# Optimization experiments

Measured on AMD Instinct MI355X. Metric: run time of the kernel, lower is better.

Reference implementation:

```python
import jax, jax.numpy as jnp
import numpy as np

WS = 8       # window_size
SHIFT = 4    # shift_size
NH = 6       # num_heads
C = 192      # dim
EPS = 1e-5


def _rel_index(ws):
    # standard Swin relative position index, [ws*ws, ws*ws]
    coords = np.stack(np.meshgrid(np.arange(ws), np.arange(ws), indexing='ij')).reshape(2, -1)
    rel = coords[:, :, None] - coords[:, None, :]            # [2, N, N]
    rel = rel.transpose(1, 2, 0) + (ws - 1)                  # shift to >= 0
    return rel[..., 0] * (2 * ws - 1) + rel[..., 1]          # [N, N]


def _attn_mask(h, w, ws, shift):
    # shifted-window attention mask, [nW, N, N] with 0 / -100
    img = np.zeros((h, w), dtype=np.float32)
    cnt = 0
    for hs in (slice(0, -ws), slice(-ws, -shift), slice(-shift, None)):
        for wsl in (slice(0, -ws), slice(-ws, -shift), slice(-shift, None)):
            img[hs, wsl] = cnt
            cnt += 1
    mw = img.reshape(h // ws, ws, w // ws, ws).transpose(0, 2, 1, 3).reshape(-1, ws * ws)
    diff = mw[:, None, :] - mw[:, :, None]
    return np.where(diff != 0, -100.0, 0.0).astype(np.float32)


def _ln(x, g, b):
    m = x.mean(-1, keepdims=True)
    v = ((x - m) ** 2).mean(-1, keepdims=True)
    return (x - m) / jnp.sqrt(v + EPS) * g + b


def setup_inputs() -> dict:
    key = jax.random.key(0)
    ks = jax.random.split(key, 16)
    B, H, W = 32, 64, 64
    Ch = 4 * C
    s = 0.02
    return {
        'x': jax.random.normal(ks[0], (B, H * W, C), jnp.float32),
        'h': H,
        'w': W,
        'norm1_g': jnp.ones((C,), jnp.float32),
        'norm1_b': jnp.zeros((C,), jnp.float32),
        'qkv_w': jax.random.normal(ks[1], (3 * C, C), jnp.float32) * s,
        'qkv_b': jnp.zeros((3 * C,), jnp.float32),
        'rpb_table': jax.random.normal(ks[2], ((2 * WS - 1) ** 2, NH), jnp.float32) * s,
        'proj_w': jax.random.normal(ks[3], (C, C), jnp.float32) * s,
        'proj_b': jnp.zeros((C,), jnp.float32),
        'norm2_g': jnp.ones((C,), jnp.float32),
        'norm2_b': jnp.zeros((C,), jnp.float32),
        'fc1_w': jax.random.normal(ks[4], (Ch, C), jnp.float32) * s,
        'fc1_b': jnp.zeros((Ch,), jnp.float32),
        'fc2_w': jax.random.normal(ks[5], (C, Ch), jnp.float32) * s,
        'fc2_b': jnp.zeros((C,), jnp.float32),
    }


def reference(x, h, w, norm1_g, norm1_b, qkv_w, qkv_b, rpb_table, proj_w, proj_b,
              norm2_g, norm2_b, fc1_w, fc1_b, fc2_w, fc2_b):
    B, L, _ = x.shape
    N = WS * WS
    hd = C // NH
    scale = hd ** -0.5
    nW = (h // WS) * (w // WS)

    shortcut = x
    xn = _ln(x, norm1_g, norm1_b).reshape(B, h, w, C)
    xs = jnp.roll(xn, (-SHIFT, -SHIFT), (1, 2))
    # window partition -> [B*nW, N, C]
    xw = xs.reshape(B, h // WS, WS, w // WS, WS, C).transpose(0, 1, 3, 2, 4, 5).reshape(-1, N, C)

    qkv = (xw @ qkv_w.T + qkv_b).reshape(-1, N, 3, NH, hd).transpose(2, 0, 3, 1, 4)
    q, k, v = qkv[0], qkv[1], qkv[2]                          # [B*nW, NH, N, hd]
    attn = jnp.einsum('whnd,whmd->whnm', q * scale, k)        # [B*nW, NH, N, N]
    bias = rpb_table[jnp.asarray(_rel_index(WS))].transpose(2, 0, 1)  # [NH, N, N]
    attn = attn + bias[None]
    mask = jnp.asarray(_attn_mask(h, w, WS, SHIFT))           # [nW, N, N]
    attn = attn.reshape(B, nW, NH, N, N) + mask[None, :, None]
    attn = jax.nn.softmax(attn.reshape(-1, NH, N, N), axis=-1)
    out = jnp.einsum('whnm,whmd->whnd', attn, v).transpose(0, 2, 1, 3).reshape(-1, N, C)
    out = out @ proj_w.T + proj_b

    # window reverse + unroll
    out = out.reshape(B, h // WS, w // WS, WS, WS, C).transpose(0, 1, 3, 2, 4, 5).reshape(B, h, w, C)
    out = jnp.roll(out, (SHIFT, SHIFT), (1, 2)).reshape(B, h * w, C)

    x = shortcut + out
    xn = _ln(x, norm2_g, norm2_b)
    mlp = jax.nn.gelu(xn @ fc1_w.T + fc1_b, approximate=False) @ fc2_w.T + fc2_b
    return x + mlp
```

## Files before the change

kernel.cpp:

```cpp
#include <hip/hip_runtime.h>
#include <hip/hip_bf16.h>
#include <math.h>

typedef __bf16 bf16;
typedef __bf16 bf16x8 __attribute__((ext_vector_type(8)));
typedef float f32x4 __attribute__((ext_vector_type(4)));

typedef const __attribute__((address_space(1))) char gchar;
typedef __attribute__((address_space(3))) char lchar;

#define BATCH 32
#define HW 64
#define L 4096
#define CDIM 192
#define NHEADS 6
#define HD 32
#define NTOK 131072
#define QKVC 576
#define CH 768

template <bool PERM, typename TIN>
__global__ __launch_bounds__(256) void ln_kernel(const TIN* __restrict__ xin,
                                                 const float* __restrict__ g,
                                                 const float* __restrict__ bta,
                                                 bf16* __restrict__ yout) {
  int wave = threadIdx.x >> 6;
  int lane = threadIdx.x & 63;
  int tok = blockIdx.x * 4 + wave;
  int src;
  if (PERM) {
    int win = tok >> 6;
    int n = tok & 63;
    int bb = win >> 6;
    int wid = win & 63;
    int i = ((wid >> 3) << 3) + (n >> 3);
    int j = ((wid & 7) << 3) + (n & 7);
    int sh = (i + 4) & 63;
    int sw = (j + 4) & 63;
    src = bb * L + sh * HW + sw;
  } else {
    src = tok;
  }
  const TIN* sp = xin + (size_t)src * CDIM;
  float v0 = (float)sp[lane];
  float v1 = (float)sp[lane + 64];
  float v2 = (float)sp[lane + 128];
  float s = v0 + v1 + v2;
#pragma unroll
  for (int off = 32; off; off >>= 1) s += __shfl_xor(s, off, 64);
  float mean = s * (1.0f / 192.0f);
  float d0 = v0 - mean, d1 = v1 - mean, d2 = v2 - mean;
  float q = d0 * d0 + d1 * d1 + d2 * d2;
#pragma unroll
  for (int off = 32; off; off >>= 1) q += __shfl_xor(q, off, 64);
  float rstd = rsqrtf(q * (1.0f / 192.0f) + 1e-5f);
  bf16* dp = yout + (size_t)tok * CDIM;
  dp[lane]       = (bf16)(d0 * rstd * g[lane]       + bta[lane]);
  dp[lane + 64]  = (bf16)(d1 * rstd * g[lane + 64]  + bta[lane + 64]);
  dp[lane + 128] = (bf16)(d2 * rstd * g[lane + 128] + bta[lane + 128]);
}

template <int EPI, typename TR, typename TO>
__global__ __launch_bounds__(256) void gemm_bt(const bf16* __restrict__ A,
                                               const float* __restrict__ W,
                                               const float* __restrict__ bias,
                                               const TR* __restrict__ res,
                                               TO* __restrict__ Cout,
                                               int M, int N, int K, int ldw) {
  __shared__ alignas(16) bf16 As[128 * 32];
  __shared__ alignas(16) bf16 Bs[64 * 32];
  const int n0 = blockIdx.x * 64;
  const int m0 = blockIdx.y * 128;
  const int tid = threadIdx.x;
  const int lane = tid & 63;
  const int wave = tid >> 6;
  const int wm = (wave >> 1) * 64;
  const int wn = (wave & 1) * 32;
  const int lr = lane & 15;
  const int quad = lane >> 4;

  f32x4 acc[4][2];
#pragma unroll
  for (int i = 0; i < 4; i++)
#pragma unroll
    for (int j = 0; j < 2; j++) acc[i][j] = (f32x4){0.f, 0.f, 0.f, 0.f};

  const int arow = tid >> 2;
  const int akq = (tid & 3) * 8;

  for (int k0 = 0; k0 < K; k0 += 32) {
    const bf16* Ap = A + (size_t)(m0 + arow) * K + k0 + akq;
    *(uint4*)(&As[arow * 32 + akq]) = *(const uint4*)Ap;
    *(uint4*)(&As[(arow + 64) * 32 + akq]) = *(const uint4*)(Ap + (size_t)64 * K);
    const float* Wp = W + (size_t)(n0 + arow) * ldw + k0 + akq;
    float4 w0 = *(const float4*)Wp;
    float4 w1 = *(const float4*)(Wp + 4);
    bf16x8 bw;
    bw[0] = (bf16)w0.x; bw[1] = (bf16)w0.y; bw[2] = (bf16)w0.z; bw[3] = (bf16)w0.w;
    bw[4] = (bf16)w1.x; bw[5] = (bf16)w1.y; bw[6] = (bf16)w1.z; bw[7] = (bf16)w1.w;
    *(bf16x8*)(&Bs[arow * 32 + akq]) = bw;
    __syncthreads();

    bf16x8 af[4], bfr[2];
#pragma unroll
    for (int mi = 0; mi < 4; mi++)
      af[mi] = *(const bf16x8*)(&As[(wm + mi * 16 + lr) * 32 + quad * 8]);
#pragma unroll
    for (int nj = 0; nj < 2; nj++)
      bfr[nj] = *(const bf16x8*)(&Bs[(wn + nj * 16 + lr) * 32 + quad * 8]);
#pragma unroll
    for (int mi = 0; mi < 4; mi++)
#pragma unroll
      for (int nj = 0; nj < 2; nj++)
        acc[mi][nj] = __builtin_amdgcn_mfma_f32_16x16x32_bf16(af[mi], bfr[nj],
                                                              acc[mi][nj], 0, 0, 0);
    __syncthreads();
  }

#pragma unroll
  for (int mi = 0; mi < 4; mi++) {
#pragma unroll
    for (int nj = 0; nj < 2; nj++) {
      int col = n0 + wn + nj * 16 + lr;
      float bv = bias[col];
#pragma unroll
      for (int r = 0; r < 4; r++) {
        int row = m0 + wm + mi * 16 + quad * 4 + r;
        float v = acc[mi][nj][r] + bv;
        size_t didx;
        if (EPI == 3) {
          int win = row >> 6, n = row & 63;
          int bb = win >> 6, wid = win & 63;
          int i = ((wid >> 3) << 3) + (n >> 3);
          int j = ((wid & 7) << 3) + (n & 7);
          int fi = (i + 4) & 63;
          int fj = (j + 4) & 63;
          didx = ((size_t)(bb * L + fi * HW + fj)) * (size_t)N + col;
          v += (float)res[didx];
        } else {
          didx = (size_t)row * N + col;
        }
        Cout[didx] = (TO)v;
      }
    }
  }
}

__device__ __forceinline__ int region64(int h) {
  return (h < 56) ? 0 : ((h < 60) ? 1 : 2);
}

__global__ __launch_bounds__(64) void attn_kernel(const bf16* __restrict__ qkv,
                                                  const float* __restrict__ rpb,
                                                  bf16* __restrict__ out) {
  __shared__ alignas(16) bf16 Qs[64 * 32];
  __shared__ alignas(16) bf16 Ks[64 * 32];
  __shared__ alignas(16) bf16 Vt[32 * 64];
  __shared__ alignas(16) bf16 Ps[64 * 64];
  const int win = blockIdx.x;
  const int head = blockIdx.y;
  const int lane = threadIdx.x;
  const int lr = lane & 15;
  const int quad = lane >> 4;
  const int wid = win & 63;
  const int wi = wid >> 3, wj = wid & 7;

  const bf16* base = qkv + (size_t)win * 64 * QKVC + head * HD;
#pragma unroll
  for (int rep = 0; rep < 4; rep++) {
    int r = (lane >> 2) + rep * 16;
    int c = (lane & 3) * 8;
    *(uint4*)(&Qs[r * 32 + c]) = *(const uint4*)(base + (size_t)r * QKVC + c);
    *(uint4*)(&Ks[r * 32 + c]) = *(const uint4*)(base + CDIM + (size_t)r * QKVC + c);
    uint4 vv = *(const uint4*)(base + 2 * CDIM + (size_t)r * QKVC + c);
    bf16x8 v8 = __builtin_bit_cast(bf16x8, vv);
#pragma unroll
    for (int j = 0; j < 8; j++) Vt[(c + j) * 64 + r] = v8[j];
  }
  __syncthreads();

  f32x4 s[4][4];
  {
    bf16x8 qf[4], kf[4];
#pragma unroll
    for (int mi = 0; mi < 4; mi++)
      qf[mi] = *(const bf16x8*)(&Qs[(mi * 16 + lr) * 32 + quad * 8]);
#pragma unroll
    for (int nj = 0; nj < 4; nj++)
      kf[nj] = *(const bf16x8*)(&Ks[(nj * 16 + lr) * 32 + quad * 8]);
#pragma unroll
    for (int mi = 0; mi < 4; mi++)
#pragma unroll
      for (int nj = 0; nj < 4; nj++)
        s[mi][nj] = __builtin_amdgcn_mfma_f32_16x16x32_bf16(
            qf[mi], kf[nj], (f32x4){0.f, 0.f, 0.f, 0.f}, 0, 0, 0);
  }

  const float scale = 0.17677669529663687f;
#pragma unroll
  for (int mi = 0; mi < 4; mi++) {
#pragma unroll
    for (int nj = 0; nj < 4; nj++) {
#pragma unroll
      for (int r = 0; r < 4; r++) {
        int rr = mi * 16 + quad * 4 + r;
        int cc = nj * 16 + lr;
        int qi = rr >> 3, qj = rr & 7, ki = cc >> 3, kj = cc & 7;
        int idx = (qi - ki + 7) * 15 + (qj - kj + 7);
        float bv = rpb[idx * NHEADS + head];
        int regr = 3 * region64(wi * 8 + qi) + region64(wj * 8 + qj);
        int regc = 3 * region64(wi * 8 + ki) + region64(wj * 8 + kj);
        float mv = (regr != regc) ? -100.0f : 0.0f;
        s[mi][nj][r] = s[mi][nj][r] * scale + bv + mv;
      }
    }
  }

#pragma unroll
  for (int mi = 0; mi < 4; mi++) {
#pragma unroll
    for (int r = 0; r < 4; r++) {
      float mx = s[mi][0][r];
#pragma unroll
      for (int nj = 1; nj < 4; nj++) mx = fmaxf(mx, s[mi][nj][r]);
#pragma unroll
      for (int off = 1; off < 16; off <<= 1) mx = fmaxf(mx, __shfl_xor(mx, off, 64));
      float sum = 0.f;
#pragma unroll
      for (int nj = 0; nj < 4; nj++) {
        float p = __expf(s[mi][nj][r] - mx);
        s[mi][nj][r] = p;
        sum += p;
      }
#pragma unroll
      for (int off = 1; off < 16; off <<= 1) sum += __shfl_xor(sum, off, 64);
      float inv = 1.0f / sum;
#pragma unroll
      for (int nj = 0; nj < 4; nj++) s[mi][nj][r] *= inv;
    }
  }

#pragma unroll
  for (int mi = 0; mi < 4; mi++)
#pragma unroll
    for (int nj = 0; nj < 4; nj++)
#pragma unroll
      for (int r = 0; r < 4; r++)
        Ps[(mi * 16 + quad * 4 + r) * 64 + nj * 16 + lr] = (bf16)s[mi][nj][r];
  __syncthreads();

  f32x4 o[4][2];
#pragma unroll
  for (int mi = 0; mi < 4; mi++)
#pragma unroll
    for (int nj = 0; nj < 2; nj++) o[mi][nj] = (f32x4){0.f, 0.f, 0.f, 0.f};
#pragma unroll
  for (int ks = 0; ks < 2; ks++) {
    bf16x8 pf[4], vf[2];
#pragma unroll
    for (int mi = 0; mi < 4; mi++)
      pf[mi] = *(const bf16x8*)(&Ps[(mi * 16 + lr) * 64 + ks * 32 + quad * 8]);
#pragma unroll
    for (int nj = 0; nj < 2; nj++)
      vf[nj] = *(const bf16x8*)(&Vt[(nj * 16 + lr) * 64 + ks * 32 + quad * 8]);
#pragma unroll
    for (int mi = 0; mi < 4; mi++)
#pragma unroll
      for (int nj = 0; nj < 2; nj++)
        o[mi][nj] = __builtin_amdgcn_mfma_f32_16x16x32_bf16(pf[mi], vf[nj],
                                                            o[mi][nj], 0, 0, 0);
  }

#pragma unroll
  for (int mi = 0; mi < 4; mi++)
#pragma unroll
    for (int nj = 0; nj < 2; nj++)
#pragma unroll
      for (int r = 0; r < 4; r++) {
        size_t row = (size_t)win * 64 + mi * 16 + quad * 4 + r;
        int col = head * HD + nj * 16 + lr;
        out[row * CDIM + col] = (bf16)o[mi][nj][r];
      }
}

__global__ __launch_bounds__(256) void wconv_kernel(const float* __restrict__ fc1w,
                                                    const float* __restrict__ fc2w,
                                                    bf16* __restrict__ W1b,
                                                    bf16* __restrict__ W2b) {
  int i = blockIdx.x * 256 + threadIdx.x;
  {
    int h = i / 192;
    int cc = i - h * 192;
    int gs = cc >> 3, e = cc & 7;
    int g = (gs & ~7) | ((gs & 7) ^ (h & 7));
    W1b[i] = (bf16)fc1w[h * 192 + g * 8 + e];
  }
  {
    int c = i / 12288;
    int rem = i - c * 12288;
    int n = rem >> 6;
    int cc = rem & 63;
    int gs = cc >> 3, e = cc & 7;
    int g = gs ^ (n & 7);
    W2b[i] = (bf16)fc2w[n * 768 + c * 64 + g * 8 + e];
  }
}

__global__ __launch_bounds__(512, 4) void mlp_fused(
    const bf16* __restrict__ Xn,
    const bf16* __restrict__ W1b,
    const bf16* __restrict__ W2b,
    const float* __restrict__ b1,
    const float* __restrict__ b2,
    const bf16* __restrict__ X1,
    float* __restrict__ out) {
  __shared__ alignas(16) bf16 W1s[64 * 192];
  __shared__ alignas(16) bf16 W2s[192 * 64];
  __shared__ alignas(16) bf16 Hs[8][16 * 64];

  const int tid = threadIdx.x;
  const int lane = tid & 63;
  const int wave = tid >> 6;
  const int lr = lane & 15;
  const int quad = lane >> 4;
  const int m0 = blockIdx.x * 128;
  const int arow = m0 + wave * 16 + lr;

  bf16x8 aF[6];
  {
    const bf16* ap = Xn + (size_t)arow * CDIM + quad * 8;
#pragma unroll
    for (int ks = 0; ks < 6; ks++)
      aF[ks] = *(const bf16x8*)(ap + ks * 32);
  }

  f32x4 oacc[12];
#pragma unroll
  for (int nt = 0; nt < 12; nt++) oacc[nt] = (f32x4){0.f, 0.f, 0.f, 0.f};

  for (int c = 0; c < 12; c++) {
    const int h0 = c * 64;
    {
      const size_t cb = (size_t)c * 24576;
      const int off = wave * 1024 + lane * 16;
      const char* g1 = (const char*)W1b + cb + off;
      const char* g2 = (const char*)W2b + cb + off;
      char* l1 = (char*)W1s + wave * 1024;
      char* l2 = (char*)W2s + wave * 1024;
#pragma unroll
      for (int i = 0; i < 3; i++) {
        __builtin_amdgcn_global_load_lds((gchar*)(g1 + i * 8192),
                                         (lchar*)(l1 + i * 8192), 16, 0, 0);
        __builtin_amdgcn_global_load_lds((gchar*)(g2 + i * 8192),
                                         (lchar*)(l2 + i * 8192), 16, 0, 0);
      }
    }
    __syncthreads();

    f32x4 hacc[4];
#pragma unroll
    for (int nj = 0; nj < 4; nj++) hacc[nj] = (f32x4){0.f, 0.f, 0.f, 0.f};
#pragma unroll
    for (int ks = 0; ks < 6; ks++) {
      int c8 = ks * 4 + quad;
      int base = (c8 & ~7) | ((c8 & 7) ^ (lr & 7));
#pragma unroll
      for (int nj = 0; nj < 4; nj++) {
        bf16x8 bF = *(const bf16x8*)(&W1s[(nj * 16 + lr) * 192 + base * 8]);
        hacc[nj] = __builtin_amdgcn_mfma_f32_16x16x32_bf16(aF[ks], bF, hacc[nj], 0, 0, 0);
      }
    }

#pragma unroll
    for (int nj = 0; nj < 4; nj++) {
      float bh = b1[h0 + nj * 16 + lr];
#pragma unroll
      for (int r = 0; r < 4; r++) {
        float h = hacc[nj][r] + bh;
        float x = fabsf(h) * 0.70710678118654752f;
        float t = __fdividef(1.0f, fmaf(0.3275911f, x, 1.0f));
        float p = t * (0.254829592f +
                  t * (-0.284496736f +
                  t * (1.421413741f +
                  t * (-1.453152027f + t * 1.061405429f))));
        float er = fmaf(-p, __expf(-x * x), 1.0f);
        er = copysignf(er, h);
        float gl = 0.5f * h * (1.0f + er);
        int hr = quad * 4 + r;
        int col = nj * 16 + lr;
        int c8 = col >> 3;
        int c8s = c8 ^ (hr & 7);
        Hs[wave][hr * 64 + c8s * 8 + (col & 7)] = (bf16)gl;
      }
    }

#pragma unroll
    for (int ks = 0; ks < 2; ks++) {
      int c8 = ks * 4 + quad;
      int c8s = c8 ^ (lr & 7);
      bf16x8 hF = *(const bf16x8*)(&Hs[wave][lr * 64 + c8s * 8]);
#pragma unroll
      for (int nt = 0; nt < 12; nt++) {
        bf16x8 wF = *(const bf16x8*)(&W2s[(nt * 16 + lr) * 64 + c8s * 8]);
        oacc[nt] = __builtin_amdgcn_mfma_f32_16x16x32_bf16(hF, wF, oacc[nt], 0, 0, 0);
      }
    }
    __syncthreads();
  }

#pragma unroll
  for (int nt = 0; nt < 12; nt++) {
    float fb = b2[nt * 16 + lr];
#pragma unroll
    for (int r = 0; r < 4; r++) {
      size_t row = (size_t)(m0 + wave * 16 + quad * 4 + r);
      size_t idx = row * CDIM + nt * 16 + lr;
      out[idx] = oacc[nt][r] + fb + (float)X1[idx];
    }
  }
}

extern "C" void kernel_launch(void* const* d_in, const int* in_sizes, int n_in,
                              void* d_out, int out_size, void* d_ws, size_t ws_size,
                              hipStream_t stream) {
  const float* x      = (const float*)d_in[0];
  const float* n1g    = (const float*)d_in[3];
  const float* n1b    = (const float*)d_in[4];
  const float* qkv_w  = (const float*)d_in[5];
  const float* qkv_b  = (const float*)d_in[6];
  const float* rpb    = (const float*)d_in[7];
  const float* proj_w = (const float*)d_in[8];
  const float* proj_b = (const float*)d_in[9];
  const float* n2g    = (const float*)d_in[10];
  const float* n2b    = (const float*)d_in[11];
  const float* fc1_w  = (const float*)d_in[12];
  const float* fc1_b  = (const float*)d_in[13];
  const float* fc2_w  = (const float*)d_in[14];
  const float* fc2_b  = (const float*)d_in[15];
  float* out = (float*)d_out;

  char* wsb = (char*)d_ws;
  bf16* Q   = (bf16*)wsb;
  bf16* X1  = (bf16*)wsb;
  bf16* W1b = (bf16*)(wsb + 52428800ull);
  bf16* W2b = (bf16*)(wsb + 52428800ull + 294912ull);
  bf16* T   = (bf16*)(wsb + 150994944ull);

  ln_kernel<true, float><<<32768, 256, 0, stream>>>(x, n1g, n1b, T);
  gemm_bt<0, float, bf16><<<dim3(9, 1024), 256, 0, stream>>>(
      T, qkv_w, qkv_b, nullptr, Q, NTOK, QKVC, CDIM, CDIM);
  attn_kernel<<<dim3(2048, 6), 64, 0, stream>>>(Q, rpb, T);
  gemm_bt<3, float, bf16><<<dim3(3, 1024), 256, 0, stream>>>(
      T, proj_w, proj_b, x, X1, NTOK, CDIM, CDIM, CDIM);
  wconv_kernel<<<576, 256, 0, stream>>>(fc1_w, fc2_w, W1b, W2b);
  ln_kernel<false, bf16><<<32768, 256, 0, stream>>>(X1, n2g, n2b, T);
  mlp_fused<<<1024, 512, 0, stream>>>(T, W1b, W2b, fc1_b, fc2_b, X1, out);
}
```

Measured before the change: 584.1 us.

## Fuse LayerNorm2 into MLP kernel, remap GEMM blocks, alias attention LDS buffers

Drops the separate second LayerNorm launch by computing per-row mean/variance inside the fused MLP kernel from the bf16 residual rows held in registers, then normalizing into the MFMA A-fragments. This removes a full read/write pass of the normalized activation tensor. The GEMM block index is also permuted so consecutive blocks land on strided tiles, which may help L2/XCD locality. Attention shared memory is cut by aliasing the probability buffer onto the Q/K buffers, which could raise occupancy but relies on Q/K being dead before P is written.

```diff
diff --git a/kernel.cpp b/kernel.cpp
--- a/kernel.cpp
+++ b/kernel.cpp
@@ -69,8 +69,13 @@
                                                int M, int N, int K, int ldw) {
   __shared__ alignas(16) bf16 As[128 * 32];
   __shared__ alignas(16) bf16 Bs[64 * 32];
-  const int n0 = blockIdx.x * 64;
-  const int m0 = blockIdx.y * 128;
+  const int gx = gridDim.x;
+  const int nb = gx * gridDim.y;
+  const int id = blockIdx.y * gx + blockIdx.x;
+  const int per = nb >> 3;
+  const int jj = ((id & 7) * per) + (id >> 3);
+  const int n0 = (jj % gx) * 64;
+  const int m0 = (jj / gx) * 128;
   const int tid = threadIdx.x;
   const int lane = tid & 63;
   const int wave = tid >> 6;
@@ -153,10 +158,11 @@
 __global__ __launch_bounds__(64) void attn_kernel(const bf16* __restrict__ qkv,
                                                   const float* __restrict__ rpb,
                                                   bf16* __restrict__ out) {
-  __shared__ alignas(16) bf16 Qs[64 * 32];
-  __shared__ alignas(16) bf16 Ks[64 * 32];
+  __shared__ alignas(16) bf16 QKP[64 * 64];
   __shared__ alignas(16) bf16 Vt[32 * 64];
-  __shared__ alignas(16) bf16 Ps[64 * 64];
+  bf16* Qs = QKP;
+  bf16* Ks = QKP + 64 * 32;
+  bf16* Ps = QKP;
   const int win = blockIdx.x;
   const int head = blockIdx.y;
   const int lane = threadIdx.x;
@@ -307,16 +313,18 @@
 }
 
 __global__ __launch_bounds__(512, 4) void mlp_fused(
-    const bf16* __restrict__ Xn,
+    const bf16* __restrict__ X1,
+    const float* __restrict__ g2,
+    const float* __restrict__ bt2,
     const bf16* __restrict__ W1b,
     const bf16* __restrict__ W2b,
     const float* __restrict__ b1,
     const float* __restrict__ b2,
-    const bf16* __restrict__ X1,
     float* __restrict__ out) {
   __shared__ alignas(16) bf16 W1s[64 * 192];
   __shared__ alignas(16) bf16 W2s[192 * 64];
   __shared__ alignas(16) bf16 Hs[8][16 * 64];
+  __shared__ float Gs[192], Bn[192];
 
   const int tid = threadIdx.x;
   const int lane = tid & 63;
@@ -326,12 +334,38 @@
   const int m0 = blockIdx.x * 128;
   const int arow = m0 + wave * 16 + lr;
 
+  if (tid < 192) { Gs[tid] = g2[tid]; Bn[tid] = bt2[tid]; }
+  __syncthreads();
+
+  bf16x8 xr[6];
+  {
+    const bf16* xp = X1 + (size_t)arow * CDIM + quad * 8;
+#pragma unroll
+    for (int ks = 0; ks < 6; ks++) xr[ks] = *(const bf16x8*)(xp + ks * 32);
+  }
+  float s1 = 0.f, s2 = 0.f;
+#pragma unroll
+  for (int ks = 0; ks < 6; ks++)
+#pragma unroll
+    for (int j = 0; j < 8; j++) {
+      float v = (float)xr[ks][j];
+      s1 += v;
+      s2 = fmaf(v, v, s2);
+    }
+  s1 += __shfl_xor(s1, 16, 64); s1 += __shfl_xor(s1, 32, 64);
+  s2 += __shfl_xor(s2, 16, 64); s2 += __shfl_xor(s2, 32, 64);
+  float mean = s1 * (1.0f / 192.0f);
+  float var = fmaxf(s2 * (1.0f / 192.0f) - mean * mean, 0.0f);
+  float rstd = rsqrtf(var + 1e-5f);
   bf16x8 aF[6];
-  {
-    const bf16* ap = Xn + (size_t)arow * CDIM + quad * 8;
-#pragma unroll
-    for (int ks = 0; ks < 6; ks++)
-      aF[ks] = *(const bf16x8*)(ap + ks * 32);
+#pragma unroll
+  for (int ks = 0; ks < 6; ks++) {
+    int cb = ks * 32 + quad * 8;
+    bf16x8 a;
+#pragma unroll
+    for (int j = 0; j < 8; j++)
+      a[j] = (bf16)(((float)xr[ks][j] - mean) * rstd * Gs[cb + j] + Bn[cb + j]);
+    aF[ks] = a;
   }
 
   f32x4 oacc[12];
@@ -344,14 +378,14 @@
       const size_t cb = (size_t)c * 24576;
       const int off = wave * 1024 + lane * 16;
       const char* g1 = (const char*)W1b + cb + off;
-      const char* g2 = (const char*)W2b + cb + off;
+      const char* gg2 = (const char*)W2b + cb + off;
       char* l1 = (char*)W1s + wave * 1024;
       char* l2 = (char*)W2s + wave * 1024;
 #pragma unroll
       for (int i = 0; i < 3; i++) {
         __builtin_amdgcn_global_load_lds((gchar*)(g1 + i * 8192),
                                          (lchar*)(l1 + i * 8192), 16, 0, 0);
-        __builtin_amdgcn_global_load_lds((gchar*)(g2 + i * 8192),
+        __builtin_amdgcn_global_load_lds((gchar*)(gg2 + i * 8192),
                                          (lchar*)(l2 + i * 8192), 16, 0, 0);
       }
     }
@@ -453,6 +487,5 @@
   gemm_bt<3, float, bf16><<<dim3(3, 1024), 256, 0, stream>>>(
       T, proj_w, proj_b, x, X1, NTOK, CDIM, CDIM, CDIM);
   wconv_kernel<<<576, 256, 0, stream>>>(fc1_w, fc2_w, W1b, W2b);
-  ln_kernel<false, bf16><<<32768, 256, 0, stream>>>(X1, n2g, n2b, T);
-  mlp_fused<<<1024, 512, 0, stream>>>(T, W1b, W2b, fc1_b, fc2_b, X1, out);
-}
+  mlp_fused<<<1024, 512, 0, stream>>>(X1, n2g, n2b, W1b, W2b, fc1_b, fc2_b, out);
+}
```

Result: faster. 537.5 us (-8.0%).
